# Kernel optimization log

Measured on AMD Instinct MI355X. Metric: run time of the kernel, lower is better.

## Reference

```python
import jax, jax.numpy as jnp
import numpy as np

# Model dims (GatedAttentionLayer of Qwen3.5 ANE hybrid stack)
C = 2048      # hidden_size
H = 16        # num_attention_heads
HK = 4        # num_key_value_heads
D = 128       # head_dim
ROT = 32      # rotary_dim = head_dim * partial_rotary_factor (0.25)
S = 1024      # sequence length (prefill)
CTX = 1024    # kv cache context length
N_ATTN = 6    # number of full-attention layers -> kv_cache leading dim 2*N_ATTN
EPS = 1e-6
ROPE_THETA = 1e7


def _rotate_half(x):
    h = x.shape[-1] // 2
    return jnp.concatenate([-x[..., h:], x[..., :h]], axis=-1)


def _rms_norm(x, w, eps=EPS):
    # Qwen3.5 convention: stored weight is (w - 1), applied as (1 + weight)
    r = jax.lax.rsqrt(jnp.mean(x * x, axis=-1, keepdims=True) + eps)
    return x * r * (1.0 + w)


def setup_inputs() -> dict:
    key = jax.random.key(0)
    ks = jax.random.split(key, 6)
    hidden_states = jax.random.normal(ks[0], (1, C, 1, S), jnp.float32)
    q_proj_w = jax.random.normal(ks[1], (H * 2 * D, C), jnp.float32) * 0.02  # q + gate
    k_proj_w = jax.random.normal(ks[2], (HK * D, C), jnp.float32) * 0.02
    v_proj_w = jax.random.normal(ks[3], (HK * D, C), jnp.float32) * 0.02
    o_proj_w = jax.random.normal(ks[4], (C, H * D), jnp.float32) * 0.02
    q_norm_w = jnp.zeros((D,), jnp.float32)
    k_norm_w = jnp.zeros((D,), jnp.float32)
    kv_cache = jnp.zeros((2 * N_ATTN, HK, CTX, D), jnp.float32)
    position_ids = jnp.arange(S, dtype=jnp.int32)
    # causal mask: 0 on/below diagonal, -1e9 above
    causal_mask = jnp.where(
        jnp.arange(CTX)[None, :] <= jnp.arange(S)[:, None], 0.0, -1e9
    ).astype(jnp.float32)[None, None]  # [1,1,S,CTX]
    # RoPE tables over rotary_dim
    inv_freq = 1.0 / (ROPE_THETA ** (jnp.arange(0, ROT, 2, dtype=jnp.float32) / ROT))
    t = jnp.arange(CTX, dtype=jnp.float32)
    freqs = jnp.outer(t, inv_freq)          # [CTX, ROT//2]
    emb = jnp.concatenate([freqs, freqs], -1)  # [CTX, ROT]
    cos_cached = jnp.cos(emb)
    sin_cached = jnp.sin(emb)
    return dict(hidden_states=hidden_states, q_proj_w=q_proj_w, k_proj_w=k_proj_w,
                v_proj_w=v_proj_w, o_proj_w=o_proj_w, q_norm_w=q_norm_w,
                k_norm_w=k_norm_w, kv_cache=kv_cache, causal_mask=causal_mask,
                position_ids=position_ids, cos_cached=cos_cached,
                sin_cached=sin_cached, attn_layer_idx=0)


def reference(hidden_states, q_proj_w, k_proj_w, v_proj_w, o_proj_w,
              q_norm_w, k_norm_w, kv_cache, causal_mask, position_ids,
              cos_cached, sin_cached, attn_layer_idx):
    x = hidden_states[0, :, 0, :]                     # [C, S]
    q_raw = q_proj_w @ x                              # [H*2D, S]  (1x1 Conv2d == GEMM)
    qg = q_raw.reshape(H, 2 * D, S)
    q = jnp.transpose(qg[:, :D, :], (0, 2, 1))        # [H, S, D]
    gate = jnp.transpose(qg[:, D:, :], (0, 2, 1))     # [H, S, D]
    k = jnp.transpose((k_proj_w @ x).reshape(HK, D, S), (0, 2, 1))  # [HK, S, D]
    v = jnp.transpose((v_proj_w @ x).reshape(HK, D, S), (0, 2, 1))  # [HK, S, D]

    q = _rms_norm(q, q_norm_w)
    k = _rms_norm(k, k_norm_w)

    cos = cos_cached[position_ids]   # [S, ROT]
    sin = sin_cached[position_ids]

    def rope(t):
        rot, pas = t[..., :ROT], t[..., ROT:]
        rot = rot * cos + _rotate_half(rot) * sin
        return jnp.concatenate([rot, pas], axis=-1)

    q, k = rope(q), rope(k)

    # prefill cache write at pos_start = position_ids[0]
    k_idx = 2 * attn_layer_idx
    v_idx = k_idx + 1
    pos_start = position_ids[0]
    kv_cache = jax.lax.dynamic_update_slice(kv_cache, k[None], (k_idx, 0, pos_start, 0))
    kv_cache = jax.lax.dynamic_update_slice(kv_cache, v[None], (v_idx, 0, pos_start, 0))

    g = H // HK  # GQA repeat (expand+reshape == contiguous repeat)
    k_full = jnp.repeat(kv_cache[k_idx], g, axis=0)   # [H, CTX, D]
    v_full = jnp.repeat(kv_cache[v_idx], g, axis=0)   # [H, CTX, D]

    scale = D ** -0.5
    attn = jnp.einsum('hsd,htd->hst', q, k_full) * scale + causal_mask[0]
    attn = jax.nn.softmax(attn, axis=-1)
    out = jnp.einsum('hst,htd->hsd', attn, v_full)    # [H, S, D]
    out = out * jax.nn.sigmoid(gate)
    out = jnp.transpose(out, (0, 2, 1)).reshape(H * D, S)
    output = (o_proj_w @ out)[None, :, None, :]       # [1, C, 1, S]
    return output
```

## Files before the change

kernel.cpp:

```cpp
#include <hip/hip_runtime.h>
#include <cstdint>

#define S_LEN 1024
#define C_DIM 2048
#define NH    16
#define NHK   4
#define HD    128
#define ROT   32
#define SCALE 0.08838834764831845f

typedef __bf16 bf16x8 __attribute__((ext_vector_type(8)));
typedef float floatx4 __attribute__((ext_vector_type(4)));
typedef float floatx8 __attribute__((ext_vector_type(8)));
typedef float floatx16 __attribute__((ext_vector_type(16)));
typedef unsigned short ushortx8 __attribute__((ext_vector_type(8)));

__device__ __forceinline__ unsigned short f2bf(float f) {
  union { float f; uint32_t u; } x; x.f = f;
  uint32_t r = (x.u + 0x7fffu + ((x.u >> 16) & 1u)) >> 16;
  return (unsigned short)r;
}
__device__ __forceinline__ float bf2f(unsigned short v) {
  union { uint32_t u; float f; } x; x.u = (uint32_t)v << 16; return x.f;
}
__device__ __forceinline__ ushortx8 cvt8(floatx8 v) {
  ushortx8 o;
#pragma unroll
  for (int j = 0; j < 8; ++j) o[j] = f2bf(v[j]);
  return o;
}

__device__ __forceinline__ void async_copy16(const unsigned short* g, unsigned short* l) {
  __builtin_amdgcn_global_load_lds(
      (const __attribute__((address_space(1))) void*)g,
      (__attribute__((address_space(3))) void*)l,
      16, 0, 0);
}

#define WAIT_VM(N) asm volatile("s_waitcnt vmcnt(" #N ")" ::: "memory")

__device__ __forceinline__ void bar_lds_only() {
  asm volatile("s_waitcnt lgkmcnt(0)" ::: "memory");
  __builtin_amdgcn_s_barrier();
}

__global__ __launch_bounds__(256)
void transpose_cast_x_kernel(const float* __restrict__ x, unsigned short* __restrict__ xT) {
  __shared__ float t[32][33];
  int st = blockIdx.x, ct = blockIdx.y;
  int c = threadIdx.x & 31, rq = threadIdx.x >> 5;
#pragma unroll
  for (int i = 0; i < 4; ++i) {
    int r = rq + i * 8;
    t[r][c] = x[(size_t)(ct * 32 + r) * S_LEN + st * 32 + c];
  }
  __syncthreads();
#pragma unroll
  for (int i = 0; i < 4; ++i) {
    int r = rq + i * 8;
    xT[(size_t)(st * 32 + r) * C_DIM + ct * 32 + c] = f2bf(t[c][r]);
  }
}

__device__ __forceinline__ void norm_rope_epi(
    floatx16 (&acc)[2], float (*pp)[32],
    const float* __restrict__ w, const int* __restrict__ pos_ids,
    const float* __restrict__ cosc, const float* __restrict__ sinc,
    unsigned short* __restrict__ outp,
    int wave, int lane, int wm, int scol0) {
  int l31 = lane & 31, half = lane >> 5;
  float s = 0.f;
#pragma unroll
  for (int mi = 0; mi < 2; ++mi)
#pragma unroll
    for (int reg = 0; reg < 16; ++reg) { float v = acc[mi][reg]; s += v * v; }
  s += __shfl_xor(s, 32);
  if (half == 0) pp[wave][l31] = s;
  __syncthreads();
  float rn = rsqrtf((pp[wave][l31] + pp[wave ^ 1][l31]) * (1.0f / 128.0f) + 1e-6f);
  int scol = scol0 + l31;
  int pos = pos_ids[scol];
#pragma unroll
  for (int mi = 0; mi < 2; ++mi) {
    bool rope = (wm == 0) && (mi == 0);
#pragma unroll
    for (int g = 0; g < 4; ++g) {
      int dbase = wm + mi * 32 + half * 4 + g * 8;
      ushort4 o;
#pragma unroll
      for (int rr = 0; rr < 4; ++rr) {
        int reg = g * 4 + rr;
        int d = dbase + rr;
        float v = acc[mi][reg] * rn * (1.0f + w[d]);
        if (rope) {
          float cv = cosc[pos * ROT + d], sv = sinc[pos * ROT + d];
          int d2 = (d < 16) ? d + 16 : d - 16;
          float pv = acc[mi][reg ^ 8] * rn * (1.0f + w[d2]);
          v = v * cv + ((d < 16) ? -pv : pv) * sv;
        }
        ((unsigned short*)&o)[rr] = f2bf(v);
      }
      *(ushort4*)&outp[(size_t)scol * HD + dbase] = o;
    }
  }
}

#define MFMA_PHASE(BUF)                                                            \
  {                                                                                \
    _Pragma("unroll")                                                              \
    for (int kb = 0; kb < 4; ++kb) {                                               \
      int co = (((kb << 1) | half) ^ (l31 & 7)) << 3;                              \
      bf16x8 a0 = *(const bf16x8*)&Asm[BUF][(wm + l31) * 64 + co];                 \
      bf16x8 a1 = *(const bf16x8*)&Asm[BUF][(wm + 32 + l31) * 64 + co];            \
      bf16x8 bf = *(const bf16x8*)&Bsm[BUF][(wn + l31) * 64 + co];                 \
      acc[0] = __builtin_amdgcn_mfma_f32_32x32x16_bf16(a0, bf, acc[0], 0, 0, 0);   \
      acc[1] = __builtin_amdgcn_mfma_f32_32x32x16_bf16(a1, bf, acc[1], 0, 0, 0);   \
    }                                                                              \
  }

__global__ __launch_bounds__(256, 4)
void gemm_qkv_fused(const float* __restrict__ qpw, const float* __restrict__ kpw,
                    const float* __restrict__ vpw,
                    const unsigned short* __restrict__ BT,
                    const float* __restrict__ qnw, const float* __restrict__ knw,
                    const int* __restrict__ pos_ids,
                    const float* __restrict__ cosc, const float* __restrict__ sinc,
                    unsigned short* __restrict__ qb, unsigned short* __restrict__ kbuf,
                    unsigned short* __restrict__ vTb, unsigned short* __restrict__ sgb) {
  __shared__ unsigned short Asm[2][128 * 64];
  __shared__ unsigned short Bsm[2][64 * 64];
  __shared__ float pp[4][32];
  int tid = threadIdx.x, wave = tid >> 6, lane = tid & 63;
  int l31 = lane & 31, half = lane >> 5;
  int wm = (wave & 1) * 64, wn = (wave >> 1) * 32;
  int m0 = blockIdx.x * 128, n0 = blockIdx.y * 64;
  int r8 = lane >> 3, c8 = lane & 7;
  int arow[4], brow[2], apos[4], bpos[2];
#pragma unroll
  for (int i = 0; i < 4; ++i) { arow[i] = wave * 32 + i * 8 + r8; apos[i] = c8 ^ (arow[i] & 7); }
#pragma unroll
  for (int i = 0; i < 2; ++i) { brow[i] = wave * 16 + i * 8 + r8; bpos[i] = c8 ^ (brow[i] & 7); }
  int ty = blockIdx.x;
  const float* Agf;
  if (ty < 32)      Agf = qpw + (size_t)m0 * C_DIM;
  else if (ty < 36) Agf = kpw + (size_t)(m0 - 4096) * C_DIM;
  else              Agf = vpw + (size_t)(m0 - 4608) * C_DIM;
  const unsigned short* Bg = BT + (size_t)n0 * C_DIM;
  floatx16 acc[2];
  acc[0] = (floatx16)0.f; acc[1] = (floatx16)0.f;
  floatx8 fA[4]; ushortx8 rB[2];

#pragma unroll
  for (int i = 0; i < 4; ++i) fA[i] = *(const floatx8*)(Agf + (size_t)arow[i] * C_DIM + c8 * 8);
#pragma unroll
  for (int i = 0; i < 2; ++i) rB[i] = *(const ushortx8*)(Bg + (size_t)brow[i] * C_DIM + c8 * 8);
#pragma unroll
  for (int i = 0; i < 4; ++i) *(ushortx8*)&Asm[0][arow[i] * 64 + apos[i] * 8] = cvt8(fA[i]);
#pragma unroll
  for (int i = 0; i < 2; ++i) *(ushortx8*)&Bsm[0][brow[i] * 64 + bpos[i] * 8] = rB[i];
  bar_lds_only();

  for (int t = 0; t < 32; ++t) {
    int b = t & 1;
    if (t < 31) {
      int kt = (t + 1) * 64;
#pragma unroll
      for (int i = 0; i < 4; ++i) fA[i] = *(const floatx8*)(Agf + (size_t)arow[i] * C_DIM + kt + c8 * 8);
#pragma unroll
      for (int i = 0; i < 2; ++i) rB[i] = *(const ushortx8*)(Bg + (size_t)brow[i] * C_DIM + kt + c8 * 8);
    }
    if (b == 0) { MFMA_PHASE(0) } else { MFMA_PHASE(1) }
    if (t < 31) {
#pragma unroll
      for (int i = 0; i < 4; ++i) *(ushortx8*)&Asm[b ^ 1][arow[i] * 64 + apos[i] * 8] = cvt8(fA[i]);
#pragma unroll
      for (int i = 0; i < 2; ++i) *(ushortx8*)&Bsm[b ^ 1][brow[i] * 64 + bpos[i] * 8] = rB[i];
    }
    bar_lds_only();
  }

  int scol0 = n0 + wn;
  if (ty < 32) {
    int h = ty >> 1;
    if ((ty & 1) == 0) {
      norm_rope_epi(acc, pp, qnw, pos_ids, cosc, sinc,
                    qb + (size_t)h * S_LEN * HD, wave, lane, wm, scol0);
    } else {
      int scol = scol0 + l31;
#pragma unroll
      for (int mi = 0; mi < 2; ++mi)
#pragma unroll
        for (int g = 0; g < 4; ++g) {
          int dbase = wm + mi * 32 + half * 4 + g * 8;
          ushort4 o;
#pragma unroll
          for (int rr = 0; rr < 4; ++rr)
            ((unsigned short*)&o)[rr] = f2bf(1.0f / (1.0f + __expf(-acc[mi][g * 4 + rr])));
          *(ushort4*)&sgb[((size_t)h * S_LEN + scol) * HD + dbase] = o;
        }
    }
  } else if (ty < 36) {
    int hk = ty - 32;
    norm_rope_epi(acc, pp, knw, pos_ids, cosc, sinc,
                  kbuf + (size_t)hk * S_LEN * HD, wave, lane, wm, scol0);
  } else {
    int hk = ty - 36;
#pragma unroll
    for (int mi = 0; mi < 2; ++mi)
#pragma unroll
      for (int reg = 0; reg < 16; ++reg) {
        int d = wm + mi * 32 + (reg & 3) + 8 * (reg >> 2) + 4 * half;
        vTb[(size_t)hk * HD * S_LEN + (size_t)d * S_LEN + scol0 + l31] = f2bf(acc[mi][reg]);
      }
  }
}

__global__ __launch_bounds__(256, 4)
void gemm_oproj(const float* __restrict__ A,
                const unsigned short* __restrict__ BT,
                float* __restrict__ C) {
  __shared__ unsigned short Asm[2][128 * 64];
  __shared__ unsigned short Bsm[2][64 * 64];
  int tid = threadIdx.x, wave = tid >> 6, lane = tid & 63;
  int l31 = lane & 31, half = lane >> 5;
  int wm = (wave & 1) * 64, wn = (wave >> 1) * 32;
  int m0 = blockIdx.x * 128, n0 = blockIdx.y * 64;
  int r8 = lane >> 3, c8 = lane & 7;
  int arow[4], brow[2], apos[4], bpos[2];
#pragma unroll
  for (int i = 0; i < 4; ++i) { arow[i] = wave * 32 + i * 8 + r8; apos[i] = c8 ^ (arow[i] & 7); }
#pragma unroll
  for (int i = 0; i < 2; ++i) { brow[i] = wave * 16 + i * 8 + r8; bpos[i] = c8 ^ (brow[i] & 7); }
  const float* Ag = A + (size_t)m0 * C_DIM;
  const unsigned short* Bg = BT + (size_t)n0 * C_DIM;
  floatx16 acc[2];
  acc[0] = (floatx16)0.f; acc[1] = (floatx16)0.f;
  floatx8 fA[4]; ushortx8 rB[2];

#pragma unroll
  for (int i = 0; i < 4; ++i) fA[i] = *(const floatx8*)(Ag + (size_t)arow[i] * C_DIM + c8 * 8);
#pragma unroll
  for (int i = 0; i < 2; ++i) rB[i] = *(const ushortx8*)(Bg + (size_t)brow[i] * C_DIM + c8 * 8);
#pragma unroll
  for (int i = 0; i < 4; ++i) *(ushortx8*)&Asm[0][arow[i] * 64 + apos[i] * 8] = cvt8(fA[i]);
#pragma unroll
  for (int i = 0; i < 2; ++i) *(ushortx8*)&Bsm[0][brow[i] * 64 + bpos[i] * 8] = rB[i];
  bar_lds_only();

  for (int t = 0; t < 32; ++t) {
    int b = t & 1;
    if (t < 31) {
      int kt = (t + 1) * 64;
#pragma unroll
      for (int i = 0; i < 4; ++i) fA[i] = *(const floatx8*)(Ag + (size_t)arow[i] * C_DIM + kt + c8 * 8);
#pragma unroll
      for (int i = 0; i < 2; ++i) rB[i] = *(const ushortx8*)(Bg + (size_t)brow[i] * C_DIM + kt + c8 * 8);
    }
    if (b == 0) { MFMA_PHASE(0) } else { MFMA_PHASE(1) }
    if (t < 31) {
#pragma unroll
      for (int i = 0; i < 4; ++i) *(ushortx8*)&Asm[b ^ 1][arow[i] * 64 + apos[i] * 8] = cvt8(fA[i]);
#pragma unroll
      for (int i = 0; i < 2; ++i) *(ushortx8*)&Bsm[b ^ 1][brow[i] * 64 + bpos[i] * 8] = rB[i];
    }
    bar_lds_only();
  }
#pragma unroll
  for (int mi = 0; mi < 2; ++mi)
#pragma unroll
    for (int reg = 0; reg < 16; ++reg) {
      int row = m0 + wm + mi * 32 + (reg & 3) + 8 * (reg >> 2) + 4 * half;
      C[(size_t)row * S_LEN + n0 + wn + l31] = acc[mi][reg];
    }
}

__global__ __launch_bounds__(256)
void attn_kernel(const unsigned short* __restrict__ qb,
                 const unsigned short* __restrict__ kbuf,
                 const unsigned short* __restrict__ vTb,
                 const unsigned short* __restrict__ sgb,
                 unsigned short* __restrict__ outT) {
  __shared__ __align__(16) unsigned short Ks[2][64 * 128];
  __shared__ __align__(16) unsigned short Vs[128 * 64];
  __shared__ __align__(16) unsigned short Ps[4][16][72];
  int h = blockIdx.x, qt = blockIdx.y;
  int s0 = qt * 64;
  int hk = h >> 2;
  int tid = threadIdx.x, wave = tid >> 6, lane = tid & 63;
  int l16 = lane & 15, quad = lane >> 4;
  int lsw = l16 & 7;

  const unsigned short* qg = qb + ((size_t)(h * S_LEN + s0 + wave * 16 + l16)) * HD;
  bf16x8 qfr[4];
#pragma unroll
  for (int kb = 0; kb < 4; ++kb)
    qfr[kb] = *(const bf16x8*)(qg + kb * 32 + quad * 8);
  asm volatile("" :: "v"(qfr[0]), "v"(qfr[1]), "v"(qfr[2]), "v"(qfr[3]));
  WAIT_VM(0);

  float m_r[4], l_r[4];
#pragma unroll
  for (int r = 0; r < 4; ++r) { m_r[r] = -1e30f; l_r[r] = 0.f; }
  floatx4 acc_o[8];
#pragma unroll
  for (int i = 0; i < 8; ++i) acc_o[i] = (floatx4)0.f;
  int srow_base = s0 + wave * 16 + quad * 4;

  const unsigned short* kg0 = kbuf + (size_t)hk * S_LEN * HD;
  const unsigned short* vg0 = vTb + (size_t)hk * HD * S_LEN;

  int kr4 = lane >> 4, kc16 = lane & 15;
  int vr8 = lane >> 3, vc8 = lane & 7;

#define STAGE_K(BUF, T)                                                    \
  { _Pragma("unroll")                                                      \
    for (int i = 0; i < 4; ++i) {                                          \
      int rbase = wave * 16 + i * 4;                                       \
      int row = rbase + kr4;                                               \
      int cs = kc16 ^ (row & 7);                                           \
      async_copy16(kg0 + (size_t)((T) * 64 + row) * HD + cs * 8,           \
                   &Ks[BUF][rbase * 128]); } }
#define STAGE_V(T)                                                         \
  { _Pragma("unroll")                                                      \
    for (int i = 0; i < 4; ++i) {                                          \
      int rbase = wave * 32 + i * 8;                                       \
      int row = rbase + vr8;                                               \
      int cs = vc8 ^ (row & 7);                                            \
      async_copy16(vg0 + (size_t)row * S_LEN + (T) * 64 + cs * 8,          \
                   Vs + rbase * 64); } }

  STAGE_K(0, 0)
  STAGE_V(0)

  for (int t = 0; t <= qt; ++t) {
    int cur = t & 1;
    bool more = (t < qt);
    if (more) { STAGE_K(cur ^ 1, t + 1) WAIT_VM(8); }
    else      { WAIT_VM(4); }
    __builtin_amdgcn_s_barrier();

    floatx4 acc_s[4];
#pragma unroll
    for (int ni = 0; ni < 4; ++ni) acc_s[ni] = (floatx4)0.f;
#pragma unroll
    for (int kb = 0; kb < 4; ++kb) {
#pragma unroll
      for (int ni = 0; ni < 4; ++ni) {
        int cl = (kb * 4 + quad) ^ lsw;
        bf16x8 bk = *(const bf16x8*)&Ks[cur][(ni * 16 + l16) * 128 + cl * 8];
        acc_s[ni] = __builtin_amdgcn_mfma_f32_16x16x32_bf16(qfr[kb], bk, acc_s[ni], 0, 0, 0);
      }
    }

    int jt = t * 64;
    bool diag = (t == qt);
    float alpha[4];
#pragma unroll
    for (int r = 0; r < 4; ++r) {
      float scv[4];
      float mx = -1e30f;
#pragma unroll
      for (int ni = 0; ni < 4; ++ni) {
        float sv = acc_s[ni][r] * SCALE;
        if (diag) {
          int jg = jt + ni * 16 + l16;
          if (jg > srow_base + r) sv = -1e30f;
        }
        scv[ni] = sv;
        mx = fmaxf(mx, sv);
      }
#pragma unroll
      for (int off = 8; off; off >>= 1) mx = fmaxf(mx, __shfl_xor(mx, off, 16));
      float mnew = fmaxf(m_r[r], mx);
      float psv = 0.f;
#pragma unroll
      for (int ni = 0; ni < 4; ++ni) {
        float pv = (scv[ni] > -1e29f) ? __expf(scv[ni] - mnew) : 0.f;
        Ps[wave][quad * 4 + r][ni * 16 + l16] = f2bf(pv);
        psv += pv;
      }
#pragma unroll
      for (int off = 8; off; off >>= 1) psv += __shfl_xor(psv, off, 16);
      alpha[r] = __expf(m_r[r] - mnew);
      m_r[r] = mnew;
      l_r[r] = l_r[r] * alpha[r] + psv;
    }
#pragma unroll
    for (int i = 0; i < 8; ++i)
#pragma unroll
      for (int r = 0; r < 4; ++r) acc_o[i][r] *= alpha[r];

    if (more) { WAIT_VM(4); }
    else      { WAIT_VM(0); }
    __builtin_amdgcn_s_barrier();

#pragma unroll
    for (int kb2 = 0; kb2 < 2; ++kb2) {
      bf16x8 ap = *(const bf16x8*)&Ps[wave][l16][kb2 * 32 + quad * 8];
#pragma unroll
      for (int ni2 = 0; ni2 < 8; ++ni2) {
        int cl = (kb2 * 4 + quad) ^ lsw;
        bf16x8 bv = *(const bf16x8*)&Vs[(ni2 * 16 + l16) * 64 + cl * 8];
        acc_o[ni2] = __builtin_amdgcn_mfma_f32_16x16x32_bf16(ap, bv, acc_o[ni2], 0, 0, 0);
      }
    }
    __builtin_amdgcn_s_barrier();
    if (more) { STAGE_V(t + 1) }
  }

#pragma unroll
  for (int r = 0; r < 4; ++r) {
    int s = srow_base + r;
    float inv = 1.0f / l_r[r];
    const unsigned short* sgp = sgb + ((size_t)h * S_LEN + s) * HD;
    unsigned short* op = outT + (size_t)s * (NH * HD) + h * HD;
#pragma unroll
    for (int ni2 = 0; ni2 < 8; ++ni2) {
      int d = ni2 * 16 + l16;
      op[d] = f2bf(acc_o[ni2][r] * inv * bf2f(sgp[d]));
    }
  }
#undef STAGE_K
#undef STAGE_V
}

extern "C" void kernel_launch(void* const* d_in, const int* in_sizes, int n_in,
                              void* d_out, int out_size, void* d_ws, size_t ws_size,
                              hipStream_t stream) {
  const float* hs       = (const float*)d_in[0];
  const float* q_proj_w = (const float*)d_in[1];
  const float* k_proj_w = (const float*)d_in[2];
  const float* v_proj_w = (const float*)d_in[3];
  const float* o_proj_w = (const float*)d_in[4];
  const float* q_norm_w = (const float*)d_in[5];
  const float* k_norm_w = (const float*)d_in[6];
  const int*   pos_ids  = (const int*)d_in[9];
  const float* cos_c    = (const float*)d_in[10];
  const float* sin_c    = (const float*)d_in[11];
  float* out = (float*)d_out;

  char* ws = (char*)d_ws;
  unsigned short* xT   = (unsigned short*)(ws + 0);
  unsigned short* qb   = (unsigned short*)(ws + 4194304);
  unsigned short* kbuf = (unsigned short*)(ws + 8388608);
  unsigned short* vTb  = (unsigned short*)(ws + 9437184);
  unsigned short* sgb  = (unsigned short*)(ws + 10485760);
  unsigned short* aoT  = (unsigned short*)(ws + 14680064);

  transpose_cast_x_kernel<<<dim3(32, 64), 256, 0, stream>>>(hs, xT);
  gemm_qkv_fused<<<dim3(40, 16), 256, 0, stream>>>(q_proj_w, k_proj_w, v_proj_w, xT,
                                                   q_norm_w, k_norm_w,
                                                   pos_ids, cos_c, sin_c,
                                                   qb, kbuf, vTb, sgb);
  attn_kernel<<<dim3(16, 16), 256, 0, stream>>>(qb, kbuf, vTb, sgb, aoT);
  gemm_oproj<<<dim3(16, 16), 256, 0, stream>>>(o_proj_w, aoT, out);
}
```

Before: 266.6 us.

## Pre-cast weights to bf16 and load GEMM operands directly into registers

Adds a separate kernel that converts all q/k/v/o projection weights to bf16 in workspace each call. The two GEMMs then drop shared-memory staging and barriers, loading MFMA fragments straight from global memory into double-buffered registers. This removes in-loop fp32 conversion and LDS traffic, at the cost of an extra full pass over the weights and uncoalesced per-lane global reads with no on-chip reuse across waves. Occupancy is lowered to 3 blocks to fit the larger register footprint.

```diff
diff --git a/kernel.cpp b/kernel.cpp
--- a/kernel.cpp
+++ b/kernel.cpp
@@ -11,7 +11,6 @@
 
 typedef __bf16 bf16x8 __attribute__((ext_vector_type(8)));
 typedef float floatx4 __attribute__((ext_vector_type(4)));
-typedef float floatx8 __attribute__((ext_vector_type(8)));
 typedef float floatx16 __attribute__((ext_vector_type(16)));
 typedef unsigned short ushortx8 __attribute__((ext_vector_type(8)));
 
@@ -22,12 +21,6 @@
 }
 __device__ __forceinline__ float bf2f(unsigned short v) {
   union { uint32_t u; float f; } x; x.u = (uint32_t)v << 16; return x.f;
-}
-__device__ __forceinline__ ushortx8 cvt8(floatx8 v) {
-  ushortx8 o;
-#pragma unroll
-  for (int j = 0; j < 8; ++j) o[j] = f2bf(v[j]);
-  return o;
 }
 
 __device__ __forceinline__ void async_copy16(const unsigned short* g, unsigned short* l) {
@@ -39,9 +32,20 @@
 
 #define WAIT_VM(N) asm volatile("s_waitcnt vmcnt(" #N ")" ::: "memory")
 
-__device__ __forceinline__ void bar_lds_only() {
-  asm volatile("s_waitcnt lgkmcnt(0)" ::: "memory");
-  __builtin_amdgcn_s_barrier();
+__global__ void cast_all_kernel(const float* __restrict__ qw, const float* __restrict__ kw,
+                                const float* __restrict__ vw, const float* __restrict__ ow,
+                                unsigned short* __restrict__ out) {
+  const int NQ = 4096 * 2048 / 4, NK = 512 * 2048 / 4, NV = 512 * 2048 / 4;
+  int i = blockIdx.x * blockDim.x + threadIdx.x;
+  const float* src; int j;
+  if (i < NQ) { src = qw; j = i; }
+  else if (i < NQ + NK) { src = kw; j = i - NQ; }
+  else if (i < NQ + NK + NV) { src = vw; j = i - NQ - NK; }
+  else { src = ow; j = i - NQ - NK - NV; }
+  float4 v = ((const float4*)src)[j];
+  ushort4 o;
+  o.x = f2bf(v.x); o.y = f2bf(v.y); o.z = f2bf(v.z); o.w = f2bf(v.w);
+  ((ushort4*)out)[i] = o;
 }
 
 __global__ __launch_bounds__(256)
@@ -105,85 +109,57 @@
   }
 }
 
-#define MFMA_PHASE(BUF)                                                            \
-  {                                                                                \
-    _Pragma("unroll")                                                              \
-    for (int kb = 0; kb < 4; ++kb) {                                               \
-      int co = (((kb << 1) | half) ^ (l31 & 7)) << 3;                              \
-      bf16x8 a0 = *(const bf16x8*)&Asm[BUF][(wm + l31) * 64 + co];                 \
-      bf16x8 a1 = *(const bf16x8*)&Asm[BUF][(wm + 32 + l31) * 64 + co];            \
-      bf16x8 bf = *(const bf16x8*)&Bsm[BUF][(wn + l31) * 64 + co];                 \
-      acc[0] = __builtin_amdgcn_mfma_f32_32x32x16_bf16(a0, bf, acc[0], 0, 0, 0);   \
-      acc[1] = __builtin_amdgcn_mfma_f32_32x32x16_bf16(a1, bf, acc[1], 0, 0, 0);   \
-    }                                                                              \
-  }
-
-__global__ __launch_bounds__(256, 4)
-void gemm_qkv_fused(const float* __restrict__ qpw, const float* __restrict__ kpw,
-                    const float* __restrict__ vpw,
+#define LOAD_SET(S, KT)                                                    \
+  { _Pragma("unroll")                                                      \
+    for (int kb = 0; kb < 4; ++kb) {                                       \
+      fA0[S][kb] = *(const bf16x8*)(a0p + (KT) + kb * 16);                 \
+      fA1[S][kb] = *(const bf16x8*)(a1p + (KT) + kb * 16);                 \
+      fB[S][kb]  = *(const bf16x8*)(bp  + (KT) + kb * 16);                 \
+    } }
+
+#define MFMA_SET(S)                                                        \
+  { _Pragma("unroll")                                                      \
+    for (int kb = 0; kb < 4; ++kb) {                                       \
+      acc[0] = __builtin_amdgcn_mfma_f32_32x32x16_bf16(fA0[S][kb], fB[S][kb], acc[0], 0, 0, 0); \
+      acc[1] = __builtin_amdgcn_mfma_f32_32x32x16_bf16(fA1[S][kb], fB[S][kb], acc[1], 0, 0, 0); \
+    } }
+
+__global__ __launch_bounds__(256, 3)
+void gemm_qkv_fused(const unsigned short* __restrict__ A,
                     const unsigned short* __restrict__ BT,
-                    const float* __restrict__ qnw, const float* __restrict__ knw,
+                    const float* __restrict__ qw, const float* __restrict__ kw,
                     const int* __restrict__ pos_ids,
                     const float* __restrict__ cosc, const float* __restrict__ sinc,
                     unsigned short* __restrict__ qb, unsigned short* __restrict__ kbuf,
                     unsigned short* __restrict__ vTb, unsigned short* __restrict__ sgb) {
-  __shared__ unsigned short Asm[2][128 * 64];
-  __shared__ unsigned short Bsm[2][64 * 64];
   __shared__ float pp[4][32];
   int tid = threadIdx.x, wave = tid >> 6, lane = tid & 63;
   int l31 = lane & 31, half = lane >> 5;
   int wm = (wave & 1) * 64, wn = (wave >> 1) * 32;
   int m0 = blockIdx.x * 128, n0 = blockIdx.y * 64;
-  int r8 = lane >> 3, c8 = lane & 7;
-  int arow[4], brow[2], apos[4], bpos[2];
-#pragma unroll
-  for (int i = 0; i < 4; ++i) { arow[i] = wave * 32 + i * 8 + r8; apos[i] = c8 ^ (arow[i] & 7); }
-#pragma unroll
-  for (int i = 0; i < 2; ++i) { brow[i] = wave * 16 + i * 8 + r8; bpos[i] = c8 ^ (brow[i] & 7); }
-  int ty = blockIdx.x;
-  const float* Agf;
-  if (ty < 32)      Agf = qpw + (size_t)m0 * C_DIM;
-  else if (ty < 36) Agf = kpw + (size_t)(m0 - 4096) * C_DIM;
-  else              Agf = vpw + (size_t)(m0 - 4608) * C_DIM;
-  const unsigned short* Bg = BT + (size_t)n0 * C_DIM;
+  const unsigned short* a0p = A + (size_t)(m0 + wm + l31) * C_DIM + half * 8;
+  const unsigned short* a1p = A + (size_t)(m0 + wm + 32 + l31) * C_DIM + half * 8;
+  const unsigned short* bp  = BT + (size_t)(n0 + wn + l31) * C_DIM + half * 8;
   floatx16 acc[2];
   acc[0] = (floatx16)0.f; acc[1] = (floatx16)0.f;
-  floatx8 fA[4]; ushortx8 rB[2];
-
-#pragma unroll
-  for (int i = 0; i < 4; ++i) fA[i] = *(const floatx8*)(Agf + (size_t)arow[i] * C_DIM + c8 * 8);
-#pragma unroll
-  for (int i = 0; i < 2; ++i) rB[i] = *(const ushortx8*)(Bg + (size_t)brow[i] * C_DIM + c8 * 8);
-#pragma unroll
-  for (int i = 0; i < 4; ++i) *(ushortx8*)&Asm[0][arow[i] * 64 + apos[i] * 8] = cvt8(fA[i]);
-#pragma unroll
-  for (int i = 0; i < 2; ++i) *(ushortx8*)&Bsm[0][brow[i] * 64 + bpos[i] * 8] = rB[i];
-  bar_lds_only();
-
-  for (int t = 0; t < 32; ++t) {
-    int b = t & 1;
-    if (t < 31) {
-      int kt = (t + 1) * 64;
-#pragma unroll
-      for (int i = 0; i < 4; ++i) fA[i] = *(const floatx8*)(Agf + (size_t)arow[i] * C_DIM + kt + c8 * 8);
-#pragma unroll
-      for (int i = 0; i < 2; ++i) rB[i] = *(const ushortx8*)(Bg + (size_t)brow[i] * C_DIM + kt + c8 * 8);
-    }
-    if (b == 0) { MFMA_PHASE(0) } else { MFMA_PHASE(1) }
-    if (t < 31) {
-#pragma unroll
-      for (int i = 0; i < 4; ++i) *(ushortx8*)&Asm[b ^ 1][arow[i] * 64 + apos[i] * 8] = cvt8(fA[i]);
-#pragma unroll
-      for (int i = 0; i < 2; ++i) *(ushortx8*)&Bsm[b ^ 1][brow[i] * 64 + bpos[i] * 8] = rB[i];
-    }
-    bar_lds_only();
+  bf16x8 fA0[2][4], fA1[2][4], fB[2][4];
+
+  LOAD_SET(0, 0)
+  LOAD_SET(1, 64)
+
+  for (int t = 0; t < 32; t += 2) {
+    MFMA_SET(0)
+    if (t + 2 < 32) LOAD_SET(0, (t + 2) * 64)
+    MFMA_SET(1)
+    if (t + 3 < 32) LOAD_SET(1, (t + 3) * 64)
   }
 
   int scol0 = n0 + wn;
+  int ty = blockIdx.x;
   if (ty < 32) {
     int h = ty >> 1;
     if ((ty & 1) == 0) {
-      norm_rope_epi(acc, pp, qnw, pos_ids, cosc, sinc,
+      norm_rope_epi(acc, pp, qw, pos_ids, cosc, sinc,
                     qb + (size_t)h * S_LEN * HD, wave, lane, wm, scol0);
     } else {
       int scol = scol0 + l31;
@@ -201,7 +177,7 @@
     }
   } else if (ty < 36) {
     int hk = ty - 32;
-    norm_rope_epi(acc, pp, knw, pos_ids, cosc, sinc,
+    norm_rope_epi(acc, pp, kw, pos_ids, cosc, sinc,
                   kbuf + (size_t)hk * S_LEN * HD, wave, lane, wm, scol0);
   } else {
     int hk = ty - 36;
@@ -215,56 +191,31 @@
   }
 }
 
-__global__ __launch_bounds__(256, 4)
-void gemm_oproj(const float* __restrict__ A,
+__global__ __launch_bounds__(256, 3)
+void gemm_oproj(const unsigned short* __restrict__ A,
                 const unsigned short* __restrict__ BT,
                 float* __restrict__ C) {
-  __shared__ unsigned short Asm[2][128 * 64];
-  __shared__ unsigned short Bsm[2][64 * 64];
   int tid = threadIdx.x, wave = tid >> 6, lane = tid & 63;
   int l31 = lane & 31, half = lane >> 5;
   int wm = (wave & 1) * 64, wn = (wave >> 1) * 32;
   int m0 = blockIdx.x * 128, n0 = blockIdx.y * 64;
-  int r8 = lane >> 3, c8 = lane & 7;
-  int arow[4], brow[2], apos[4], bpos[2];
-#pragma unroll
-  for (int i = 0; i < 4; ++i) { arow[i] = wave * 32 + i * 8 + r8; apos[i] = c8 ^ (arow[i] & 7); }
-#pragma unroll
-  for (int i = 0; i < 2; ++i) { brow[i] = wave * 16 + i * 8 + r8; bpos[i] = c8 ^ (brow[i] & 7); }
-  const float* Ag = A + (size_t)m0 * C_DIM;
-  const unsigned short* Bg = BT + (size_t)n0 * C_DIM;
+  const unsigned short* a0p = A + (size_t)(m0 + wm + l31) * C_DIM + half * 8;
+  const unsigned short* a1p = A + (size_t)(m0 + wm + 32 + l31) * C_DIM + half * 8;
+  const unsigned short* bp  = BT + (size_t)(n0 + wn + l31) * C_DIM + half * 8;
   floatx16 acc[2];
   acc[0] = (floatx16)0.f; acc[1] = (floatx16)0.f;
-  floatx8 fA[4]; ushortx8 rB[2];
-
-#pragma unroll
-  for (int i = 0; i < 4; ++i) fA[i] = *(const floatx8*)(Ag + (size_t)arow[i] * C_DIM + c8 * 8);
-#pragma unroll
-  for (int i = 0; i < 2; ++i) rB[i] = *(const ushortx8*)(Bg + (size_t)brow[i] * C_DIM + c8 * 8);
-#pragma unroll
-  for (int i = 0; i < 4; ++i) *(ushortx8*)&Asm[0][arow[i] * 64 + apos[i] * 8] = cvt8(fA[i]);
-#pragma unroll
-  for (int i = 0; i < 2; ++i) *(ushortx8*)&Bsm[0][brow[i] * 64 + bpos[i] * 8] = rB[i];
-  bar_lds_only();
-
-  for (int t = 0; t < 32; ++t) {
-    int b = t & 1;
-    if (t < 31) {
-      int kt = (t + 1) * 64;
-#pragma unroll
-      for (int i = 0; i < 4; ++i) fA[i] = *(const floatx8*)(Ag + (size_t)arow[i] * C_DIM + kt + c8 * 8);
-#pragma unroll
-      for (int i = 0; i < 2; ++i) rB[i] = *(const ushortx8*)(Bg + (size_t)brow[i] * C_DIM + kt + c8 * 8);
-    }
-    if (b == 0) { MFMA_PHASE(0) } else { MFMA_PHASE(1) }
-    if (t < 31) {
-#pragma unroll
-      for (int i = 0; i < 4; ++i) *(ushortx8*)&Asm[b ^ 1][arow[i] * 64 + apos[i] * 8] = cvt8(fA[i]);
-#pragma unroll
-      for (int i = 0; i < 2; ++i) *(ushortx8*)&Bsm[b ^ 1][brow[i] * 64 + bpos[i] * 8] = rB[i];
-    }
-    bar_lds_only();
-  }
+  bf16x8 fA0[2][4], fA1[2][4], fB[2][4];
+
+  LOAD_SET(0, 0)
+  LOAD_SET(1, 64)
+
+  for (int t = 0; t < 32; t += 2) {
+    MFMA_SET(0)
+    if (t + 2 < 32) LOAD_SET(0, (t + 2) * 64)
+    MFMA_SET(1)
+    if (t + 3 < 32) LOAD_SET(1, (t + 3) * 64)
+  }
+
 #pragma unroll
   for (int mi = 0; mi < 2; ++mi)
 #pragma unroll
@@ -440,18 +391,20 @@
   float* out = (float*)d_out;
 
   char* ws = (char*)d_ws;
-  unsigned short* xT   = (unsigned short*)(ws + 0);
-  unsigned short* qb   = (unsigned short*)(ws + 4194304);
-  unsigned short* kbuf = (unsigned short*)(ws + 8388608);
-  unsigned short* vTb  = (unsigned short*)(ws + 9437184);
-  unsigned short* sgb  = (unsigned short*)(ws + 10485760);
-  unsigned short* aoT  = (unsigned short*)(ws + 14680064);
-
+  unsigned short* wqkv = (unsigned short*)(ws + 0);
+  unsigned short* wo   = (unsigned short*)(ws + 20971520);
+  unsigned short* xT   = (unsigned short*)(ws + 29360128);
+  unsigned short* qb   = (unsigned short*)(ws + 33554432);
+  unsigned short* kbuf = (unsigned short*)(ws + 37748736);
+  unsigned short* vTb  = (unsigned short*)(ws + 38797312);
+  unsigned short* sgb  = (unsigned short*)(ws + 39845888);
+  unsigned short* aoT  = (unsigned short*)(ws + 44040192);
+
+  cast_all_kernel<<<14336, 256, 0, stream>>>(q_proj_w, k_proj_w, v_proj_w, o_proj_w, wqkv);
   transpose_cast_x_kernel<<<dim3(32, 64), 256, 0, stream>>>(hs, xT);
-  gemm_qkv_fused<<<dim3(40, 16), 256, 0, stream>>>(q_proj_w, k_proj_w, v_proj_w, xT,
-                                                   q_norm_w, k_norm_w,
+  gemm_qkv_fused<<<dim3(40, 16), 256, 0, stream>>>(wqkv, xT, q_norm_w, k_norm_w,
                                                    pos_ids, cos_c, sin_c,
                                                    qb, kbuf, vTb, sgb);
   attn_kernel<<<dim3(16, 16), 256, 0, stream>>>(qb, kbuf, vTb, sgb, aoT);
-  gemm_oproj<<<dim3(16, 16), 256, 0, stream>>>(o_proj_w, aoT, out);
-}
+  gemm_oproj<<<dim3(16, 16), 256, 0, stream>>>(wo, aoT, out);
+}
```

Result: slower. 372.6 us (+39.7%).
